# Kernel tuning notes

Hardware: AMD Instinct MI355X
Metric: run time of the kernel (lower is better)

The kernel has to match this reference:

```python
import jax, jax.numpy as jnp
import numpy as np
from jax import lax


def setup_inputs() -> dict:
    key = jax.random.key(0)
    k1, k2 = jax.random.split(key)
    x = jax.random.normal(k1, (16, 224, 224, 256), dtype=jnp.float32)
    # Conv2D(1, 7): kernel HWIO [7,7,2,1], glorot-ish scale
    conv_w = jax.random.normal(k2, (7, 7, 2, 1), dtype=jnp.float32) * 0.1
    conv_b = jnp.zeros((1,), dtype=jnp.float32)
    return {"x": x, "conv_w": conv_w, "conv_b": conv_b}


def reference(x, conv_w, conv_b):
    # channel-wise stats: [B,H,W,1] each
    max_pool = jnp.max(x, axis=-1, keepdims=True)
    avg_pool = jnp.mean(x, axis=-1, keepdims=True)
    concat = jnp.concatenate([max_pool, avg_pool], axis=-1)  # [B,H,W,2]
    attn = lax.conv_general_dilated(
        concat, conv_w,
        window_strides=(1, 1), padding='SAME',
        dimension_numbers=('NHWC', 'HWIO', 'NHWC'))
    attn = jax.nn.sigmoid(attn + conv_b)  # [B,H,W,1]
    return x * attn
```

## Files before the change

### kernel.cpp

```cpp
#include <hip/hip_runtime.h>
#include <math.h>

#define B_ 16
#define H_ 224
#define W_ 224
#define C_ 256
#define NPIX (B_*H_*W_)

__global__ __launch_bounds__(256) void pool_kernel(const float* __restrict__ x,
                                                   float2* __restrict__ pooled) {
    const int wave = threadIdx.x >> 6;
    const int lane = threadIdx.x & 63;
    const int pid  = blockIdx.x * 4 + wave;
    const float4* px = (const float4*)(x + (size_t)pid * C_);
    float4 v = px[lane];
    float m = fmaxf(fmaxf(v.x, v.y), fmaxf(v.z, v.w));
    float s = v.x + v.y + v.z + v.w;
    #pragma unroll
    for (int off = 1; off < 64; off <<= 1) {
        m = fmaxf(m, __shfl_xor(m, off));
        s += __shfl_xor(s, off);
    }
    if (lane == 0) pooled[pid] = make_float2(m, s * (1.0f / 256.0f));
}

__global__ __launch_bounds__(256) void attn_mul_kernel(const float* __restrict__ x,
                                                       const float2* __restrict__ pooled,
                                                       const float* __restrict__ cw,
                                                       const float* __restrict__ cb,
                                                       float* __restrict__ out) {
    __shared__ float sw[98];
    __shared__ float sbias;
    __shared__ float sattn[64];
    const int t = threadIdx.x;
    if (t < 98) sw[t] = cw[t];
    if (t == 98) sbias = cb[0];
    __syncthreads();

    const int p   = t >> 2;
    const int s   = t & 3;
    const int pid = blockIdx.x * 64 + p;
    const int b   = pid / (H_ * W_);
    const int rem = pid % (H_ * W_);
    const int h   = rem / W_;
    const int w   = rem % W_;

    float acc = 0.0f;
    #pragma unroll
    for (int tap = 0; tap < 49; tap += 4) {
        const int tp = tap + s;
        if (tp < 49) {
            const int kh = tp / 7, kw = tp % 7;
            const int hh = h + kh - 3, ww = w + kw - 3;
            if (hh >= 0 && hh < H_ && ww >= 0 && ww < W_) {
                const float2 pv = pooled[((size_t)b * H_ + hh) * W_ + ww];
                acc = fmaf(pv.x, sw[tp * 2],     acc);
                acc = fmaf(pv.y, sw[tp * 2 + 1], acc);
            }
        }
    }
    acc += __shfl_xor(acc, 1);
    acc += __shfl_xor(acc, 2);
    if (s == 0) sattn[p] = 1.0f / (1.0f + expf(-(acc + sbias)));
    __syncthreads();

    const float4* xx = (const float4*)(x   + (size_t)blockIdx.x * 64 * C_);
    float4*       oo = (float4*)      (out + (size_t)blockIdx.x * 64 * C_);
    #pragma unroll
    for (int i = 0; i < 16; ++i) {
        const int idx = i * 256 + t;
        const float a = sattn[idx >> 6];
        float4 v = xx[idx];
        v.x *= a; v.y *= a; v.z *= a; v.w *= a;
        oo[idx] = v;
    }
}

extern "C" void kernel_launch(void* const* d_in, const int* in_sizes, int n_in,
                              void* d_out, int out_size, void* d_ws, size_t ws_size,
                              hipStream_t stream) {
    const float* x  = (const float*)d_in[0];
    const float* cw = (const float*)d_in[1];
    const float* cb = (const float*)d_in[2];
    float* out      = (float*)d_out;
    float2* pooled  = (float2*)d_ws;

    pool_kernel<<<NPIX / 4, 256, 0, stream>>>(x, pooled);
    attn_mul_kernel<<<NPIX / 64, 256, 0, stream>>>(x, pooled, cw, cb, out);
}
```

Baseline: 468.9 us.

## Use row-per-block attention with shared-memory pooled tile and nontemporal streaming

The attention kernel now processes one full image row per block. It stages a 7-row halo of pooled stats into shared memory and computes the 7x7 conv with one thread per pixel. The pool kernel handles four pixels per wave with 16-lane reductions. Both kernels use nontemporal loads and stores for the large tensor to reduce cache pollution. Block order is interleaved across rows, and the larger per-block work reduces the number of blocks and adds a shared-memory staging step.

```diff
diff --git a/kernel.cpp b/kernel.cpp
--- a/kernel.cpp
+++ b/kernel.cpp
@@ -6,73 +6,89 @@
 #define W_ 224
 #define C_ 256
 #define NPIX (B_*H_*W_)
+#define NROW (B_*H_)
+
+typedef float f32x4 __attribute__((ext_vector_type(4)));
 
 __global__ __launch_bounds__(256) void pool_kernel(const float* __restrict__ x,
                                                    float2* __restrict__ pooled) {
-    const int wave = threadIdx.x >> 6;
-    const int lane = threadIdx.x & 63;
-    const int pid  = blockIdx.x * 4 + wave;
-    const float4* px = (const float4*)(x + (size_t)pid * C_);
-    float4 v = px[lane];
-    float m = fmaxf(fmaxf(v.x, v.y), fmaxf(v.z, v.w));
-    float s = v.x + v.y + v.z + v.w;
+    const int t    = threadIdx.x;
+    const int wave = t >> 6;
+    const int lane = t & 63;
+    const int grp  = lane >> 4;
+    const int sub  = lane & 15;
+    const int pid  = (blockIdx.x * 4 + wave) * 4 + grp;
+    const f32x4* px = (const f32x4*)(x + (size_t)pid * C_);
+    float m = -INFINITY, s = 0.0f;
     #pragma unroll
-    for (int off = 1; off < 64; off <<= 1) {
+    for (int j = 0; j < 4; ++j) {
+        f32x4 v = __builtin_nontemporal_load(&px[j * 16 + sub]);
+        m = fmaxf(m, fmaxf(fmaxf(v.x, v.y), fmaxf(v.z, v.w)));
+        s += (v.x + v.y) + (v.z + v.w);
+    }
+    #pragma unroll
+    for (int off = 1; off < 16; off <<= 1) {
         m = fmaxf(m, __shfl_xor(m, off));
         s += __shfl_xor(s, off);
     }
-    if (lane == 0) pooled[pid] = make_float2(m, s * (1.0f / 256.0f));
+    if (sub == 0) pooled[pid] = make_float2(m, s * (1.0f / 256.0f));
 }
 
-__global__ __launch_bounds__(256) void attn_mul_kernel(const float* __restrict__ x,
+__global__ __launch_bounds__(256) void attn_row_kernel(const float* __restrict__ x,
                                                        const float2* __restrict__ pooled,
                                                        const float* __restrict__ cw,
                                                        const float* __restrict__ cb,
                                                        float* __restrict__ out) {
-    __shared__ float sw[98];
-    __shared__ float sbias;
-    __shared__ float sattn[64];
-    const int t = threadIdx.x;
-    if (t < 98) sw[t] = cw[t];
+    __shared__ float2 spool[7][232];
+    __shared__ float2 sw2[49];
+    __shared__ float  sbias;
+    __shared__ float  sattn[224];
+
+    const int t   = threadIdx.x;
+    const int bid = blockIdx.x;
+    const int row = (bid & 7) * (NROW / 8) + (bid >> 3);
+    const int b   = row / H_;
+    const int h   = row % H_;
+
+    if (t < 98)  ((float*)sw2)[t] = cw[t];
     if (t == 98) sbias = cb[0];
+
+    const float2* prow = pooled + (size_t)b * (H_ * W_);
+    for (int idx = t; idx < 7 * 230; idx += 256) {
+        const int r  = idx / 230;
+        const int ci = idx % 230;
+        const int hh = h - 3 + r;
+        const int c  = ci - 3;
+        float2 v = make_float2(0.0f, 0.0f);
+        if (hh >= 0 && hh < H_ && c >= 0 && c < W_) v = prow[hh * W_ + c];
+        spool[r][ci] = v;
+    }
     __syncthreads();
 
-    const int p   = t >> 2;
-    const int s   = t & 3;
-    const int pid = blockIdx.x * 64 + p;
-    const int b   = pid / (H_ * W_);
-    const int rem = pid % (H_ * W_);
-    const int h   = rem / W_;
-    const int w   = rem % W_;
-
-    float acc = 0.0f;
-    #pragma unroll
-    for (int tap = 0; tap < 49; tap += 4) {
-        const int tp = tap + s;
-        if (tp < 49) {
-            const int kh = tp / 7, kw = tp % 7;
-            const int hh = h + kh - 3, ww = w + kw - 3;
-            if (hh >= 0 && hh < H_ && ww >= 0 && ww < W_) {
-                const float2 pv = pooled[((size_t)b * H_ + hh) * W_ + ww];
-                acc = fmaf(pv.x, sw[tp * 2],     acc);
-                acc = fmaf(pv.y, sw[tp * 2 + 1], acc);
+    if (t < W_) {
+        float acc = 0.0f;
+        #pragma unroll
+        for (int kh = 0; kh < 7; ++kh) {
+            #pragma unroll
+            for (int kw = 0; kw < 7; ++kw) {
+                const float2 pv = spool[kh][t + kw];
+                const float2 wv = sw2[kh * 7 + kw];
+                acc = fmaf(pv.x, wv.x, fmaf(pv.y, wv.y, acc));
             }
         }
+        sattn[t] = 1.0f / (1.0f + expf(-(acc + sbias)));
     }
-    acc += __shfl_xor(acc, 1);
-    acc += __shfl_xor(acc, 2);
-    if (s == 0) sattn[p] = 1.0f / (1.0f + expf(-(acc + sbias)));
     __syncthreads();
 
-    const float4* xx = (const float4*)(x   + (size_t)blockIdx.x * 64 * C_);
-    float4*       oo = (float4*)      (out + (size_t)blockIdx.x * 64 * C_);
-    #pragma unroll
-    for (int i = 0; i < 16; ++i) {
+    const f32x4* xx = (const f32x4*)(x   + (size_t)row * W_ * C_);
+    f32x4*       oo = (f32x4*)      (out + (size_t)row * W_ * C_);
+    #pragma unroll 4
+    for (int i = 0; i < 56; ++i) {
         const int idx = i * 256 + t;
         const float a = sattn[idx >> 6];
-        float4 v = xx[idx];
+        f32x4 v = __builtin_nontemporal_load(&xx[idx]);
         v.x *= a; v.y *= a; v.z *= a; v.w *= a;
-        oo[idx] = v;
+        __builtin_nontemporal_store(v, &oo[idx]);
     }
 }
 
@@ -85,6 +101,6 @@
     float* out      = (float*)d_out;
     float2* pooled  = (float2*)d_ws;
 
-    pool_kernel<<<NPIX / 4, 256, 0, stream>>>(x, pooled);
-    attn_mul_kernel<<<NPIX / 64, 256, 0, stream>>>(x, pooled, cw, cb, out);
+    pool_kernel<<<NPIX / 16, 256, 0, stream>>>(x, pooled);
+    attn_row_kernel<<<NROW, 256, 0, stream>>>(x, pooled, cw, cb, out);
 }
```

Result: faster. 435.8 us (-7.1%).
